# Performance work log

Measured on AMD Instinct MI355X. Metric: run time of the kernel, lower is better.

## Reference

```python
import jax, jax.numpy as jnp
import numpy as np

B, S, D_MODEL = 2, 2048, 1024
N_HEADS, N_KV_HEADS, D_HEAD = 16, 4, 64
N_GROUPS = N_HEADS // N_KV_HEADS
ATTN_SCALE = 1.0 / np.sqrt(D_HEAD)  # qk_scale_factor=1.0
LOGIT_SOFTCAP = 15.0
WINDOW = 256
N_GLOBAL = 4
EPS = 1e-8


def _l2_normalize(x):
    norm = jnp.linalg.norm(x, axis=-1, keepdims=True)
    return x / (norm + EPS)


def _apply_rope(t, cos, sin):
    # t: (B, H, S, D); cos/sin: (S, D//2)
    half = t.shape[-1] // 2
    x1, x2 = t[..., :half], t[..., half:]
    c = cos[None, None, :, :]
    s = sin[None, None, :, :]
    return jnp.concatenate([x1 * c - x2 * s, x1 * s + x2 * c], axis=-1)


def _sliding_window_mask(seq_len, window, n_global):
    q = jnp.arange(seq_len)[:, None]
    k = jnp.arange(seq_len)[None, :]
    causal = k <= q
    in_window = k > q - window
    is_global = k < n_global
    return (causal & in_window | is_global)[None, None, :, :]


def setup_inputs() -> dict:
    key = jax.random.key(0)
    ks = jax.random.split(key, 7)
    x = jax.random.normal(ks[0], (B, S, D_MODEL), dtype=jnp.float32)
    # RoPE tables from standard inverse-frequency construction
    inv_freq = 1.0 / (10000.0 ** (jnp.arange(0, D_HEAD, 2, dtype=jnp.float32) / D_HEAD))
    angles = jnp.arange(S, dtype=jnp.float32)[:, None] * inv_freq[None, :]  # (S, D_HEAD//2)
    cos = jnp.cos(angles)
    sin = jnp.sin(angles)
    # causal mask supplied by caller (TransformerLM): (1,1,S,S) bool, True = attend
    mask = (jnp.arange(S)[None, :] <= jnp.arange(S)[:, None])[None, None, :, :]
    scale_in = 1.0 / np.sqrt(D_MODEL)
    Wq = jax.random.normal(ks[1], (D_MODEL, N_HEADS * D_HEAD), dtype=jnp.float32) * scale_in
    Wk = jax.random.normal(ks[2], (D_MODEL, N_KV_HEADS * D_HEAD), dtype=jnp.float32) * scale_in
    Wv = jax.random.normal(ks[3], (D_MODEL, N_KV_HEADS * D_HEAD), dtype=jnp.float32) * scale_in
    Wo = jax.random.normal(ks[4], (N_HEADS * D_HEAD, D_MODEL), dtype=jnp.float32) * (1.0 / np.sqrt(N_HEADS * D_HEAD))
    return {"x": x, "cos": cos, "sin": sin, "mask": mask, "Wq": Wq, "Wk": Wk, "Wv": Wv, "Wo": Wo}


def reference(x, cos, sin, mask, Wq, Wk, Wv, Wo):
    Bb, Ss, _ = x.shape
    q = (x @ Wq).reshape(Bb, Ss, N_HEADS, D_HEAD).transpose(0, 2, 1, 3)      # (B,H,S,D)
    k = (x @ Wk).reshape(Bb, Ss, N_KV_HEADS, D_HEAD).transpose(0, 2, 1, 3)   # (B,Hkv,S,D)
    v = (x @ Wv).reshape(Bb, Ss, N_KV_HEADS, D_HEAD).transpose(0, 2, 1, 3)
    # QK L2 normalization (in fp32)
    q = _l2_normalize(q.astype(jnp.float32)).astype(q.dtype)
    k = _l2_normalize(k.astype(jnp.float32)).astype(k.dtype)
    # RoPE
    q = _apply_rope(q, cos, sin)
    k = _apply_rope(k, cos, sin)
    # GQA: expand kv heads
    k_exp = jnp.repeat(k, N_GROUPS, axis=1)
    v_exp = jnp.repeat(v, N_GROUPS, axis=1)
    scores = jnp.einsum('bhqd,bhkd->bhqk', q.astype(jnp.float32), k_exp.astype(jnp.float32)) * ATTN_SCALE
    scores = LOGIT_SOFTCAP * jnp.tanh(scores / LOGIT_SOFTCAP)
    window_mask = _sliding_window_mask(Ss, WINDOW, N_GLOBAL)
    combined = mask & window_mask
    scores = jnp.where(combined, scores, jnp.float32(-1e9))
    weights = jax.nn.softmax(scores, axis=-1)
    context = jnp.einsum('bhqk,bhkd->bhqd', weights, v_exp.astype(jnp.float32))
    context = context.transpose(0, 2, 1, 3).reshape(Bb, Ss, N_HEADS * D_HEAD).astype(x.dtype)
    return context @ Wo
```

## Files before the change

### kernel.cpp

```cpp
#include <hip/hip_runtime.h>
#include <hip/hip_bf16.h>

#define BATCH 2
#define SLEN 2048
#define DMODEL 1024
#define NHEADS 16
#define NKV 4
#define DHEAD 64
#define WINDOW 256
#define NGLOBAL 4

typedef __attribute__((ext_vector_type(8))) short short8;
typedef __attribute__((ext_vector_type(4))) float floatx4;

__device__ __forceinline__ ushort f2bf(float f) {
    __hip_bfloat16 h = __float2bfloat16(f);
    return *reinterpret_cast<ushort*>(&h);
}
__device__ __forceinline__ float bf2f(ushort u) {
    __hip_bfloat16 h = *reinterpret_cast<__hip_bfloat16*>(&u);
    return __bfloat162float(h);
}
__device__ __forceinline__ bool is_bf16_inputs(const uint* cosu) {
    return (cosu[0] & 0xFFFFu) != 0u;
}
__device__ __forceinline__ void gload_lds16(const ushort* g, ushort* l) {
    __builtin_amdgcn_global_load_lds(
        (const __attribute__((address_space(1))) void*)g,
        (__attribute__((address_space(3))) void*)l, 16, 0, 0);
}

__global__ __launch_bounds__(256) void cvt_inputs(const void* __restrict__ x,
                                                  const void* __restrict__ cosi,
                                                  const void* __restrict__ sini,
                                                  ushort* __restrict__ xb,
                                                  float* __restrict__ cosf,
                                                  float* __restrict__ sinf,
                                                  const uint* __restrict__ cosu)
{
    const bool isbf = is_bf16_inputs(cosu);
    if (blockIdx.y == 0) {
        size_t i = (size_t)blockIdx.x * 256 + threadIdx.x;
        size_t e = i * 8;
        if (isbf) {
            *reinterpret_cast<uint4*>(xb + e) = reinterpret_cast<const uint4*>(x)[i];
        } else {
            const float* f = reinterpret_cast<const float*>(x) + e;
            ushort o[8];
#pragma unroll
            for (int j = 0; j < 8; ++j) o[j] = f2bf(f[j]);
            *reinterpret_cast<uint4*>(xb + e) = *reinterpret_cast<uint4*>(o);
        }
    } else {
        int i = blockIdx.x * 256 + threadIdx.x;
        if (i >= 2 * SLEN * 32) return;
        const void* src = (i < SLEN * 32) ? cosi : sini;
        float* dst = (i < SLEN * 32) ? cosf : sinf;
        int e = i & (SLEN * 32 - 1);
        dst[e] = isbf ? bf2f(reinterpret_cast<const ushort*>(src)[e])
                      : reinterpret_cast<const float*>(src)[e];
    }
}

__global__ __launch_bounds__(256) void prep_weights(const void* __restrict__ Wq,
                                                    const void* __restrict__ Wk,
                                                    const void* __restrict__ Wv,
                                                    const void* __restrict__ Wo,
                                                    ushort* __restrict__ Wt,
                                                    ushort* __restrict__ Wot,
                                                    const uint* __restrict__ cosu)
{
    const bool isbf = is_bf16_inputs(cosu);
    const int z = blockIdx.z;
    const void* src; ushort* dst; int C;
    if (z == 0)      { src = Wq; dst = Wt;                        C = 1024; }
    else if (z == 1) { src = Wk; dst = Wt + (size_t)1024 * 1024;  C = 256; }
    else if (z == 2) { src = Wv; dst = Wt + (size_t)1280 * 1024;  C = 256; }
    else             { src = Wo; dst = Wot;                       C = 1024; }
    const int bx = blockIdx.x * 32;
    if (bx >= C) return;
    const int by = blockIdx.y * 32;
    __shared__ ushort t[32][33];
    const int tx = threadIdx.x & 31, ty = threadIdx.x >> 5;
#pragma unroll
    for (int j = 0; j < 32; j += 8) {
        size_t idx = (size_t)(by + ty + j) * C + bx + tx;
        t[ty + j][tx] = isbf ? reinterpret_cast<const ushort*>(src)[idx]
                             : f2bf(reinterpret_cast<const float*>(src)[idx]);
    }
    __syncthreads();
#pragma unroll
    for (int j = 0; j < 32; j += 8)
        dst[(size_t)(bx + ty + j) * 1024 + by + tx] = t[tx][ty + j];
}

__global__ __launch_bounds__(256) void transpose_slab_bf16(const ushort* __restrict__ in,
                                                           ushort* __restrict__ out,
                                                           int R, int C)
{
    __shared__ ushort t[32][33];
    const ushort* ip = in + (size_t)blockIdx.z * R * C;
    ushort* op = out + (size_t)blockIdx.z * R * C;
    int bx = blockIdx.x * 32, by = blockIdx.y * 32;
    int tx = threadIdx.x & 31, ty = threadIdx.x >> 5;
#pragma unroll
    for (int j = 0; j < 32; j += 8)
        t[ty + j][tx] = ip[(size_t)(by + ty + j) * C + bx + tx];
    __syncthreads();
#pragma unroll
    for (int j = 0; j < 32; j += 8)
        op[(size_t)(bx + ty + j) * R + by + tx] = t[tx][ty + j];
}

template<int OUT_MODE>
__global__ __launch_bounds__(256) void gemm128(const ushort* __restrict__ A,
                                               const ushort* __restrict__ Bt,
                                               void* __restrict__ Cp,
                                               int M, int N, int K,
                                               const uint* __restrict__ cosu)
{
    __shared__ ushort lsA[128 * 64];
    __shared__ ushort lsB[128 * 64];
    const int tid = threadIdx.x;
    const int lane = tid & 63, w = tid >> 6;
    const int ln15 = lane & 15, quad = lane >> 4;
    const int wm = w >> 1, wn = w & 1;
    const int rm = blockIdx.y * 128, cn = blockIdx.x * 128;

    floatx4 acc[4][4];
#pragma unroll
    for (int i = 0; i < 4; ++i)
#pragma unroll
        for (int j = 0; j < 4; ++j) acc[i][j] = (floatx4){0.f, 0.f, 0.f, 0.f};

    for (int k0 = 0; k0 < K; k0 += 64) {
        __syncthreads();
#pragma unroll
        for (int i = 0; i < 4; ++i) {
            const int c = (i * 4 + w) * 64 + lane;
            const int row = c >> 3, col = (c & 7) * 8;
            gload_lds16(&A[(size_t)(rm + row) * K + k0 + col], &lsA[(i * 4 + w) * 512]);
            gload_lds16(&Bt[(size_t)(cn + row) * K + k0 + col], &lsB[(i * 4 + w) * 512]);
        }
        __syncthreads();
#pragma unroll
        for (int kk = 0; kk < 64; kk += 32) {
            short8 af[4], bf[4];
#pragma unroll
            for (int i = 0; i < 4; ++i) {
                af[i] = *reinterpret_cast<const short8*>(&lsA[(wm * 64 + i * 16 + ln15) * 64 + kk + quad * 8]);
                bf[i] = *reinterpret_cast<const short8*>(&lsB[(wn * 64 + i * 16 + ln15) * 64 + kk + quad * 8]);
            }
#pragma unroll
            for (int i = 0; i < 4; ++i)
#pragma unroll
                for (int j = 0; j < 4; ++j)
                    acc[i][j] = __builtin_amdgcn_mfma_f32_16x16x32_bf16(af[i], bf[j], acc[i][j], 0, 0, 0);
        }
    }

    const bool outbf = (OUT_MODE == 2) || is_bf16_inputs(cosu);
#pragma unroll
    for (int i = 0; i < 4; ++i) {
#pragma unroll
        for (int r = 0; r < 4; ++r) {
            const int grow = rm + wm * 64 + i * 16 + quad * 4 + r;
#pragma unroll
            for (int j = 0; j < 4; ++j) {
                const int gcol = cn + wn * 64 + j * 16 + ln15;
                if (outbf) reinterpret_cast<ushort*>(Cp)[(size_t)grow * N + gcol] = f2bf(acc[i][j][r]);
                else       reinterpret_cast<float*>(Cp)[(size_t)grow * N + gcol] = acc[i][j][r];
            }
        }
    }
}

__global__ __launch_bounds__(256) void norm_rope(const ushort* __restrict__ qkvb,
                                                 const float* __restrict__ cosf,
                                                 const float* __restrict__ sinf,
                                                 ushort* __restrict__ Qb,
                                                 ushort* __restrict__ Kg,
                                                 ushort* __restrict__ Vb)
{
    const int lane = threadIdx.x & 63;
    const int g = blockIdx.x * 4 + (threadIdx.x >> 6);
    const int hh = g % 24;
    const int s = (g / 24) & (SLEN - 1);
    const int b = g / (24 * SLEN);
    const size_t row = (size_t)(b * SLEN + s) * 1536;

    if (hh >= 20) {
        int hkv = hh - 20;
        Vb[((size_t)((b * NKV + hkv) * SLEN + s)) * 64 + lane] = qkvb[row + 1280 + hkv * 64 + lane];
        return;
    }
    const bool isq = hh < 16;
    const int col = isq ? hh * 64 : 1024 + (hh - 16) * 64;
    float v = bf2f(qkvb[row + col + lane]);
    float ss = v * v;
#pragma unroll
    for (int off = 32; off; off >>= 1) ss += __shfl_xor(ss, off, 64);
    float nv = v / (sqrtf(ss) + 1e-8f);
    float p = __shfl(nv, lane ^ 32, 64);
    int dh = lane & 31;
    float c = cosf[s * 32 + dh];
    float sn = sinf[s * 32 + dh];
    float o = (lane < 32) ? (nv * c - p * sn) : (p * sn + nv * c);
    if (isq) Qb[((size_t)((b * NHEADS + hh) * SLEN + s)) * 64 + lane] = f2bf(o);
    else {
        int hkv = hh - 16;
        Kg[((size_t)((b * NKV + hkv) * SLEN + s)) * 64 + lane] = f2bf(o);
    }
}

__global__ __launch_bounds__(256) void attn_mfma(const ushort* __restrict__ Qb,
                                                 const ushort* __restrict__ Kg,
                                                 const ushort* __restrict__ Vtg,
                                                 ushort* __restrict__ ctx)
{
    __shared__ ushort Ks[64 * 72];
    __shared__ ushort Vs[64 * 72];
    __shared__ ushort Ps[4][16 * 72];

    const int tid = threadIdx.x;
    const int lane = tid & 63, w = tid >> 6;
    const int ln15 = lane & 15, quad = lane >> 4;
    const int bid = blockIdx.x;
    const int qt = bid & 31, bh = bid >> 5;
    const int h = bh & (NHEADS - 1), b = bh >> 4, hkv = h >> 2;
    const int q0 = qt * 64;
    const int qw = q0 + w * 16;

    const ushort* Qrow = Qb + ((size_t)bh * SLEN + qw) * 64;
    const ushort* Kbase = Kg + (size_t)(b * NKV + hkv) * SLEN * 64;
    const ushort* Vbase = Vtg + (size_t)(b * NKV + hkv) * 64 * SLEN;

    short8 qf0 = *reinterpret_cast<const short8*>(Qrow + (size_t)ln15 * 64 + quad * 8);
    short8 qf1 = *reinterpret_cast<const short8*>(Qrow + (size_t)ln15 * 64 + 32 + quad * 8);

    floatx4 O0 = {0,0,0,0}, O1 = {0,0,0,0}, O2 = {0,0,0,0}, O3 = {0,0,0,0};
    float lp[4] = {0.f, 0.f, 0.f, 0.f};

    int kminA = q0 - (WINDOW - 1); if (kminA < 0) kminA = 0;
    kminA &= ~63;
    const int gmax = kminA < NGLOBAL ? kminA : NGLOBAL;
    const int nc = (q0 + 64 - kminA) >> 6;

    for (int c = (gmax > 0 ? -1 : 0); c < nc; ++c) {
        const int kbase = (c < 0) ? 0 : kminA + c * 64;
        __syncthreads();
#pragma unroll
        for (int j = 0; j < 2; ++j) {
            const int c2 = tid + j * 256;
            const int row = c2 >> 3, col = (c2 & 7) * 8;
            *reinterpret_cast<uint4*>(&Ks[row * 72 + col]) =
                *reinterpret_cast<const uint4*>(&Kbase[(size_t)(kbase + row) * 64 + col]);
            *reinterpret_cast<uint4*>(&Vs[row * 72 + col]) =
                *reinterpret_cast<const uint4*>(&Vbase[(size_t)row * SLEN + kbase + col]);
        }
        __syncthreads();

#pragma unroll
        for (int t = 0; t < 4; ++t) {
            short8 kf0 = *reinterpret_cast<const short8*>(&Ks[(t * 16 + ln15) * 72 + quad * 8]);
            short8 kf1 = *reinterpret_cast<const short8*>(&Ks[(t * 16 + ln15) * 72 + 32 + quad * 8]);
            floatx4 sc = {0,0,0,0};
            sc = __builtin_amdgcn_mfma_f32_16x16x32_bf16(qf0, kf0, sc, 0, 0, 0);
            sc = __builtin_amdgcn_mfma_f32_16x16x32_bf16(qf1, kf1, sc, 0, 0, 0);
            const int k = kbase + t * 16 + ln15;
#pragma unroll
            for (int r = 0; r < 4; ++r) {
                const int q = qw + quad * 4 + r;
                const bool valid = (c < 0) ? (k < gmax)
                                           : (k <= q && (k + WINDOW > q || k < NGLOBAL));
                float sv = sc[r] * 0.125f;
                float e2 = __expf(sv * 0.13333333f);
                float st = 15.f - 30.f * __builtin_amdgcn_rcpf(e2 + 1.f);
                ushort eb = valid ? f2bf(__expf(st)) : (ushort)0;
                Ps[w][(quad * 4 + r) * 72 + t * 16 + ln15] = eb;
                lp[r] += bf2f(eb);
            }
        }
        short8 af0 = *reinterpret_cast<const short8*>(&Ps[w][ln15 * 72 + quad * 8]);
        short8 af1 = *reinterpret_cast<const short8*>(&Ps[w][ln15 * 72 + 32 + quad * 8]);
#pragma unroll
        for (int n = 0; n < 4; ++n) {
            short8 vf0 = *reinterpret_cast<const short8*>(&Vs[(n * 16 + ln15) * 72 + quad * 8]);
            short8 vf1 = *reinterpret_cast<const short8*>(&Vs[(n * 16 + ln15) * 72 + 32 + quad * 8]);
            floatx4 On = (n == 0) ? O0 : (n == 1) ? O1 : (n == 2) ? O2 : O3;
            On = __builtin_amdgcn_mfma_f32_16x16x32_bf16(af0, vf0, On, 0, 0, 0);
            On = __builtin_amdgcn_mfma_f32_16x16x32_bf16(af1, vf1, On, 0, 0, 0);
            if (n == 0) O0 = On; else if (n == 1) O1 = On; else if (n == 2) O2 = On; else O3 = On;
        }
    }

#pragma unroll
    for (int r = 0; r < 4; ++r) {
#pragma unroll
        for (int off = 1; off < 16; off <<= 1)
            lp[r] += __shfl_xor(lp[r], off, 64);
        const float inv = __builtin_amdgcn_rcpf(lp[r]);
        const int q = qw + quad * 4 + r;
        ushort* crow = ctx + ((size_t)(b * SLEN + q)) * DMODEL + h * 64 + ln15;
        crow[0]  = f2bf(O0[r] * inv);
        crow[16] = f2bf(O1[r] * inv);
        crow[32] = f2bf(O2[r] * inv);
        crow[48] = f2bf(O3[r] * inv);
    }
}

extern "C" void kernel_launch(void* const* d_in, const int* in_sizes, int n_in,
                              void* d_out, int out_size, void* d_ws, size_t ws_size,
                              hipStream_t stream)
{
    (void)in_sizes; (void)n_in; (void)out_size; (void)ws_size;
    const void* x = d_in[0];
    const void* cosi = d_in[1];
    const void* sini = d_in[2];
    const uint* cosu = (const uint*)d_in[1];
    const void* Wq = d_in[4];
    const void* Wk = d_in[5];
    const void* Wv = d_in[6];
    const void* Wo = d_in[7];

    ushort* xb = (ushort*)d_ws;
    ushort* Wt = xb + (size_t)4096 * 1024;
    ushort* Wot = Wt + (size_t)1536 * 1024;
    float* cosf = (float*)(Wot + (size_t)1024 * 1024);
    float* sinf = cosf + (size_t)SLEN * 32;
    ushort* qkvb = (ushort*)(sinf + (size_t)SLEN * 32);
    ushort* Qbf = qkvb + (size_t)4096 * 1536;
    ushort* Kgf = Qbf + (size_t)BATCH * NHEADS * SLEN * 64;
    ushort* Vbf = Kgf + (size_t)BATCH * NKV * SLEN * 64;
    ushort* Vtg = Vbf + (size_t)BATCH * NKV * SLEN * 64;
    ushort* ctx = Vtg + (size_t)BATCH * NKV * 64 * SLEN;

    cvt_inputs<<<dim3(2048, 2), 256, 0, stream>>>(x, cosi, sini, xb, cosf, sinf, cosu);

    prep_weights<<<dim3(32, 32, 4), 256, 0, stream>>>(Wq, Wk, Wv, Wo, Wt, Wot, cosu);

    gemm128<2><<<dim3(12, 32), 256, 0, stream>>>(xb, Wt, qkvb, 4096, 1536, 1024, cosu);

    norm_rope<<<dim3(BATCH * SLEN * 24 / 4), 256, 0, stream>>>(qkvb, cosf, sinf, Qbf, Kgf, Vbf);

    transpose_slab_bf16<<<dim3(2, 64, BATCH * NKV), 256, 0, stream>>>(Vbf, Vtg, SLEN, 64);

    attn_mfma<<<dim3(BATCH * NHEADS * SLEN / 64), 256, 0, stream>>>(Qbf, Kgf, Vtg, ctx);

    gemm128<1><<<dim3(8, 32), 256, 0, stream>>>(ctx, Wot, d_out, 4096, 1024, 1024, cosu);
}
```

Measured before the change: 192.5 us.

## Split-K both projection GEMMs into two fp32 partials and reduce downstream

Both GEMMs now split K into two halves along grid z, which doubles the block count (384→768 and 256→512) so more of the GPU's compute units are busy. Each half writes fp32 partials. The QKV partials are summed inside norm_rope, which also keeps the pre-normalisation values in fp32 instead of bf16. The output projection gets a new reduce_out kernel that adds the two partials and writes bf16 or fp32. The cost is much more fp32 memory traffic (two full partial buffers written and read) plus one extra kernel launch.

Result: slower. 196.8 us (+2.2%).

```diff
diff --git a/kernel.cpp b/kernel.cpp
--- a/kernel.cpp
+++ b/kernel.cpp
@@ -112,12 +112,10 @@
         op[(size_t)(bx + ty + j) * R + by + tx] = t[tx][ty + j];
 }
 
-template<int OUT_MODE>
-__global__ __launch_bounds__(256) void gemm128(const ushort* __restrict__ A,
-                                               const ushort* __restrict__ Bt,
-                                               void* __restrict__ Cp,
-                                               int M, int N, int K,
-                                               const uint* __restrict__ cosu)
+__global__ __launch_bounds__(256) void gemm128_sk(const ushort* __restrict__ A,
+                                                  const ushort* __restrict__ Bt,
+                                                  float* __restrict__ P,
+                                                  int M, int N, int Kh)
 {
     __shared__ ushort lsA[128 * 64];
     __shared__ ushort lsB[128 * 64];
@@ -126,6 +124,8 @@
     const int ln15 = lane & 15, quad = lane >> 4;
     const int wm = w >> 1, wn = w & 1;
     const int rm = blockIdx.y * 128, cn = blockIdx.x * 128;
+    const int kbeg = blockIdx.z * Kh;
+    float* Pz = P + (size_t)blockIdx.z * M * N;
 
     floatx4 acc[4][4];
 #pragma unroll
@@ -133,14 +133,17 @@
 #pragma unroll
         for (int j = 0; j < 4; ++j) acc[i][j] = (floatx4){0.f, 0.f, 0.f, 0.f};
 
-    for (int k0 = 0; k0 < K; k0 += 64) {
+    const size_t K = blockDim.y == 1 ? 0 : 0;
+    const int Kfull = Kh * 2;
+
+    for (int k0 = kbeg; k0 < kbeg + Kh; k0 += 64) {
         __syncthreads();
 #pragma unroll
         for (int i = 0; i < 4; ++i) {
             const int c = (i * 4 + w) * 64 + lane;
             const int row = c >> 3, col = (c & 7) * 8;
-            gload_lds16(&A[(size_t)(rm + row) * K + k0 + col], &lsA[(i * 4 + w) * 512]);
-            gload_lds16(&Bt[(size_t)(cn + row) * K + k0 + col], &lsB[(i * 4 + w) * 512]);
+            gload_lds16(&A[(size_t)(rm + row) * Kfull + k0 + col], &lsA[(i * 4 + w) * 512]);
+            gload_lds16(&Bt[(size_t)(cn + row) * Kfull + k0 + col], &lsB[(i * 4 + w) * 512]);
         }
         __syncthreads();
 #pragma unroll
@@ -159,7 +162,6 @@
         }
     }
 
-    const bool outbf = (OUT_MODE == 2) || is_bf16_inputs(cosu);
 #pragma unroll
     for (int i = 0; i < 4; ++i) {
 #pragma unroll
@@ -168,14 +170,35 @@
 #pragma unroll
             for (int j = 0; j < 4; ++j) {
                 const int gcol = cn + wn * 64 + j * 16 + ln15;
-                if (outbf) reinterpret_cast<ushort*>(Cp)[(size_t)grow * N + gcol] = f2bf(acc[i][j][r]);
-                else       reinterpret_cast<float*>(Cp)[(size_t)grow * N + gcol] = acc[i][j][r];
+                Pz[(size_t)grow * N + gcol] = acc[i][j][r];
             }
         }
     }
 }
 
-__global__ __launch_bounds__(256) void norm_rope(const ushort* __restrict__ qkvb,
+__global__ __launch_bounds__(256) void reduce_out(const float* __restrict__ P,
+                                                  void* __restrict__ out,
+                                                  size_t mn4,
+                                                  const uint* __restrict__ cosu)
+{
+    const bool isbf = is_bf16_inputs(cosu);
+    size_t i = (size_t)blockIdx.x * 256 + threadIdx.x;
+    if (i >= mn4) return;
+    const size_t mn = mn4 * 4;
+    floatx4 a = *reinterpret_cast<const floatx4*>(P + i * 4);
+    floatx4 b = *reinterpret_cast<const floatx4*>(P + mn + i * 4);
+    floatx4 s = a + b;
+    if (isbf) {
+        ushort o[4];
+#pragma unroll
+        for (int j = 0; j < 4; ++j) o[j] = f2bf(s[j]);
+        reinterpret_cast<uint2*>(out)[i] = *reinterpret_cast<uint2*>(o);
+    } else {
+        reinterpret_cast<floatx4*>(out)[i] = s;
+    }
+}
+
+__global__ __launch_bounds__(256) void norm_rope(const float* __restrict__ qkvp,
                                                  const float* __restrict__ cosf,
                                                  const float* __restrict__ sinf,
                                                  ushort* __restrict__ Qb,
@@ -188,15 +211,18 @@
     const int s = (g / 24) & (SLEN - 1);
     const int b = g / (24 * SLEN);
     const size_t row = (size_t)(b * SLEN + s) * 1536;
+    const size_t MN = (size_t)4096 * 1536;
 
     if (hh >= 20) {
         int hkv = hh - 20;
-        Vb[((size_t)((b * NKV + hkv) * SLEN + s)) * 64 + lane] = qkvb[row + 1280 + hkv * 64 + lane];
+        size_t idx = row + 1280 + hkv * 64 + lane;
+        Vb[((size_t)((b * NKV + hkv) * SLEN + s)) * 64 + lane] = f2bf(qkvp[idx] + qkvp[MN + idx]);
         return;
     }
     const bool isq = hh < 16;
     const int col = isq ? hh * 64 : 1024 + (hh - 16) * 64;
-    float v = bf2f(qkvb[row + col + lane]);
+    const size_t idx = row + col + lane;
+    float v = qkvp[idx] + qkvp[MN + idx];
     float ss = v * v;
 #pragma unroll
     for (int off = 32; off; off >>= 1) ss += __shfl_xor(ss, off, 64);
@@ -328,24 +354,27 @@
     ushort* Wot = Wt + (size_t)1536 * 1024;
     float* cosf = (float*)(Wot + (size_t)1024 * 1024);
     float* sinf = cosf + (size_t)SLEN * 32;
-    ushort* qkvb = (ushort*)(sinf + (size_t)SLEN * 32);
-    ushort* Qbf = qkvb + (size_t)4096 * 1536;
+    float* qkvp = sinf + (size_t)SLEN * 32;
+    ushort* Qbf = (ushort*)(qkvp + (size_t)2 * 4096 * 1536);
     ushort* Kgf = Qbf + (size_t)BATCH * NHEADS * SLEN * 64;
     ushort* Vbf = Kgf + (size_t)BATCH * NKV * SLEN * 64;
     ushort* Vtg = Vbf + (size_t)BATCH * NKV * SLEN * 64;
     ushort* ctx = Vtg + (size_t)BATCH * NKV * 64 * SLEN;
+    float* outp = (float*)(ctx + (size_t)4096 * 1024);
 
     cvt_inputs<<<dim3(2048, 2), 256, 0, stream>>>(x, cosi, sini, xb, cosf, sinf, cosu);
 
     prep_weights<<<dim3(32, 32, 4), 256, 0, stream>>>(Wq, Wk, Wv, Wo, Wt, Wot, cosu);
 
-    gemm128<2><<<dim3(12, 32), 256, 0, stream>>>(xb, Wt, qkvb, 4096, 1536, 1024, cosu);
-
-    norm_rope<<<dim3(BATCH * SLEN * 24 / 4), 256, 0, stream>>>(qkvb, cosf, sinf, Qbf, Kgf, Vbf);
+    gemm128_sk<<<dim3(12, 32, 2), 256, 0, stream>>>(xb, Wt, qkvp, 4096, 1536, 512);
+
+    norm_rope<<<dim3(BATCH * SLEN * 24 / 4), 256, 0, stream>>>(qkvp, cosf, sinf, Qbf, Kgf, Vbf);
 
     transpose_slab_bf16<<<dim3(2, 64, BATCH * NKV), 256, 0, stream>>>(Vbf, Vtg, SLEN, 64);
 
     attn_mfma<<<dim3(BATCH * NHEADS * SLEN / 64), 256, 0, stream>>>(Qbf, Kgf, Vtg, ctx);
 
-    gemm128<1><<<dim3(8, 32), 256, 0, stream>>>(ctx, Wot, d_out, 4096, 1024, 1024, cosu);
-}
+    gemm128_sk<<<dim3(8, 32, 2), 256, 0, stream>>>(ctx, Wot, outp, 4096, 1024, 512);
+
+    reduce_out<<<dim3(4096), 256, 0, stream>>>(outp, d_out, (size_t)4096 * 1024 / 4, cosu);
+}
```

## Fuse norm/RoPE and V transpose into QKV GEMM epilogue, merge prep kernels

Applied to the files above, without the earlier changes.

Merges the input-conversion and weight-transpose kernels into a single prep launch. The QKV GEMM now uses 128x64 tiles, so each block covers exactly one head. Its epilogue applies L2 norm and RoPE for Q/K heads and writes V directly transposed, which removes the intermediate qkv buffer and two extra kernels. The output GEMM also moves to 128x64 tiles to double block count. The cost is lower per-block reuse in the GEMMs and more staging through LDS in the epilogue.

Result: faster. 166.1 us (-13.7%).

```diff
diff --git a/kernel.cpp b/kernel.cpp
--- a/kernel.cpp
+++ b/kernel.cpp
@@ -30,17 +30,25 @@
         (__attribute__((address_space(3))) void*)l, 16, 0, 0);
 }
 
-__global__ __launch_bounds__(256) void cvt_inputs(const void* __restrict__ x,
-                                                  const void* __restrict__ cosi,
-                                                  const void* __restrict__ sini,
-                                                  ushort* __restrict__ xb,
-                                                  float* __restrict__ cosf,
-                                                  float* __restrict__ sinf,
-                                                  const uint* __restrict__ cosu)
+__global__ __launch_bounds__(256) void prep_all(const void* __restrict__ x,
+                                                const void* __restrict__ cosi,
+                                                const void* __restrict__ sini,
+                                                const void* __restrict__ Wq,
+                                                const void* __restrict__ Wk,
+                                                const void* __restrict__ Wv,
+                                                const void* __restrict__ Wo,
+                                                ushort* __restrict__ xb,
+                                                float* __restrict__ cosf,
+                                                float* __restrict__ sinf,
+                                                ushort* __restrict__ Wt,
+                                                ushort* __restrict__ Wot,
+                                                const uint* __restrict__ cosu)
 {
+    __shared__ ushort t[32][33];
     const bool isbf = is_bf16_inputs(cosu);
-    if (blockIdx.y == 0) {
-        size_t i = (size_t)blockIdx.x * 256 + threadIdx.x;
+    const int bid = blockIdx.x, tid = threadIdx.x;
+    if (bid < 2048) {
+        size_t i = (size_t)bid * 256 + tid;
         size_t e = i * 8;
         if (isbf) {
             *reinterpret_cast<uint4*>(xb + e) = reinterpret_cast<const uint4*>(x)[i];
@@ -51,37 +59,25 @@
             for (int j = 0; j < 8; ++j) o[j] = f2bf(f[j]);
             *reinterpret_cast<uint4*>(xb + e) = *reinterpret_cast<uint4*>(o);
         }
-    } else {
-        int i = blockIdx.x * 256 + threadIdx.x;
-        if (i >= 2 * SLEN * 32) return;
+        return;
+    }
+    if (bid < 2560) {
+        int i = (bid - 2048) * 256 + tid;
         const void* src = (i < SLEN * 32) ? cosi : sini;
         float* dst = (i < SLEN * 32) ? cosf : sinf;
         int e = i & (SLEN * 32 - 1);
         dst[e] = isbf ? bf2f(reinterpret_cast<const ushort*>(src)[e])
                       : reinterpret_cast<const float*>(src)[e];
-    }
-}
-
-__global__ __launch_bounds__(256) void prep_weights(const void* __restrict__ Wq,
-                                                    const void* __restrict__ Wk,
-                                                    const void* __restrict__ Wv,
-                                                    const void* __restrict__ Wo,
-                                                    ushort* __restrict__ Wt,
-                                                    ushort* __restrict__ Wot,
-                                                    const uint* __restrict__ cosu)
-{
-    const bool isbf = is_bf16_inputs(cosu);
-    const int z = blockIdx.z;
-    const void* src; ushort* dst; int C;
-    if (z == 0)      { src = Wq; dst = Wt;                        C = 1024; }
-    else if (z == 1) { src = Wk; dst = Wt + (size_t)1024 * 1024;  C = 256; }
-    else if (z == 2) { src = Wv; dst = Wt + (size_t)1280 * 1024;  C = 256; }
-    else             { src = Wo; dst = Wot;                       C = 1024; }
-    const int bx = blockIdx.x * 32;
-    if (bx >= C) return;
-    const int by = blockIdx.y * 32;
-    __shared__ ushort t[32][33];
-    const int tx = threadIdx.x & 31, ty = threadIdx.x >> 5;
+        return;
+    }
+    const void* src; ushort* dst; int C, tl;
+    if (bid < 3584)      { src = Wq; dst = Wt;                       C = 1024; tl = bid - 2560; }
+    else if (bid < 3840) { src = Wk; dst = Wt + (size_t)1024 * 1024; C = 256;  tl = bid - 3584; }
+    else if (bid < 4096) { src = Wv; dst = Wt + (size_t)1280 * 1024; C = 256;  tl = bid - 3840; }
+    else                 { src = Wo; dst = Wot;                      C = 1024; tl = bid - 4096; }
+    const int nbx = C >> 5;
+    const int bx = (tl % nbx) * 32, by = (tl / nbx) * 32;
+    const int tx = tid & 31, ty = tid >> 5;
 #pragma unroll
     for (int j = 0; j < 32; j += 8) {
         size_t idx = (size_t)(by + ty + j) * C + bx + tx;
@@ -94,122 +90,117 @@
         dst[(size_t)(bx + ty + j) * 1024 + by + tx] = t[tx][ty + j];
 }
 
-__global__ __launch_bounds__(256) void transpose_slab_bf16(const ushort* __restrict__ in,
-                                                           ushort* __restrict__ out,
-                                                           int R, int C)
+__global__ __launch_bounds__(256) void gemm_qkv_nr(const ushort* __restrict__ A,
+                                                   const ushort* __restrict__ Bt,
+                                                   const float* __restrict__ cosf,
+                                                   const float* __restrict__ sinf,
+                                                   ushort* __restrict__ Qb,
+                                                   ushort* __restrict__ Kg,
+                                                   ushort* __restrict__ Vtg)
 {
-    __shared__ ushort t[32][33];
-    const ushort* ip = in + (size_t)blockIdx.z * R * C;
-    ushort* op = out + (size_t)blockIdx.z * R * C;
-    int bx = blockIdx.x * 32, by = blockIdx.y * 32;
-    int tx = threadIdx.x & 31, ty = threadIdx.x >> 5;
-#pragma unroll
-    for (int j = 0; j < 32; j += 8)
-        t[ty + j][tx] = ip[(size_t)(by + ty + j) * C + bx + tx];
-    __syncthreads();
-#pragma unroll
-    for (int j = 0; j < 32; j += 8)
-        op[(size_t)(bx + ty + j) * R + by + tx] = t[tx][ty + j];
-}
-
-template<int OUT_MODE>
-__global__ __launch_bounds__(256) void gemm128(const ushort* __restrict__ A,
-                                               const ushort* __restrict__ Bt,
-                                               void* __restrict__ Cp,
-                                               int M, int N, int K,
-                                               const uint* __restrict__ cosu)
-{
-    __shared__ ushort lsA[128 * 64];
-    __shared__ ushort lsB[128 * 64];
+    __shared__ __align__(16) ushort buf[12288];
+    ushort* lsA = buf;
+    ushort* lsB = buf + 8192;
     const int tid = threadIdx.x;
     const int lane = tid & 63, w = tid >> 6;
     const int ln15 = lane & 15, quad = lane >> 4;
-    const int wm = w >> 1, wn = w & 1;
-    const int rm = blockIdx.y * 128, cn = blockIdx.x * 128;
-
-    floatx4 acc[4][4];
-#pragma unroll
-    for (int i = 0; i < 4; ++i)
+    const int z = blockIdx.x;
+    const int rm = blockIdx.y * 128;
+    const int cn = z * 64;
+
+    floatx4 acc[2][4];
+#pragma unroll
+    for (int i = 0; i < 2; ++i)
 #pragma unroll
         for (int j = 0; j < 4; ++j) acc[i][j] = (floatx4){0.f, 0.f, 0.f, 0.f};
 
-    for (int k0 = 0; k0 < K; k0 += 64) {
+    for (int k0 = 0; k0 < 1024; k0 += 64) {
         __syncthreads();
 #pragma unroll
         for (int i = 0; i < 4; ++i) {
             const int c = (i * 4 + w) * 64 + lane;
             const int row = c >> 3, col = (c & 7) * 8;
-            gload_lds16(&A[(size_t)(rm + row) * K + k0 + col], &lsA[(i * 4 + w) * 512]);
-            gload_lds16(&Bt[(size_t)(cn + row) * K + k0 + col], &lsB[(i * 4 + w) * 512]);
+            gload_lds16(&A[(size_t)(rm + row) * 1024 + k0 + col], &lsA[(i * 4 + w) * 512]);
+        }
+#pragma unroll
+        for (int i = 0; i < 2; ++i) {
+            const int c = (w * 2 + i) * 64 + lane;
+            const int row = c >> 3, col = (c & 7) * 8;
+            gload_lds16(&Bt[(size_t)(cn + row) * 1024 + k0 + col], &lsB[(w * 2 + i) * 512]);
         }
         __syncthreads();
 #pragma unroll
         for (int kk = 0; kk < 64; kk += 32) {
-            short8 af[4], bf[4];
-#pragma unroll
-            for (int i = 0; i < 4; ++i) {
-                af[i] = *reinterpret_cast<const short8*>(&lsA[(wm * 64 + i * 16 + ln15) * 64 + kk + quad * 8]);
-                bf[i] = *reinterpret_cast<const short8*>(&lsB[(wn * 64 + i * 16 + ln15) * 64 + kk + quad * 8]);
+            short8 af[2], bv[4];
+#pragma unroll
+            for (int i = 0; i < 2; ++i)
+                af[i] = *reinterpret_cast<const short8*>(&lsA[(w * 32 + i * 16 + ln15) * 64 + kk + quad * 8]);
+#pragma unroll
+            for (int j = 0; j < 4; ++j)
+                bv[j] = *reinterpret_cast<const short8*>(&lsB[(j * 16 + ln15) * 64 + kk + quad * 8]);
+#pragma unroll
+            for (int i = 0; i < 2; ++i)
+#pragma unroll
+                for (int j = 0; j < 4; ++j)
+                    acc[i][j] = __builtin_amdgcn_mfma_f32_16x16x32_bf16(af[i], bv[j], acc[i][j], 0, 0, 0);
+        }
+    }
+
+    __syncthreads();
+    const int b = rm >> 11, s0 = rm & (SLEN - 1);
+
+    if (z < 20) {
+#pragma unroll
+        for (int i = 0; i < 2; ++i) {
+#pragma unroll
+            for (int r = 0; r < 4; ++r) {
+                const int row_l = w * 32 + i * 16 + quad * 4 + r;
+                float v0 = acc[i][0][r], v1 = acc[i][1][r], v2 = acc[i][2][r], v3 = acc[i][3][r];
+                float ss = v0 * v0 + v1 * v1 + v2 * v2 + v3 * v3;
+                ss += __shfl_xor(ss, 1, 64);
+                ss += __shfl_xor(ss, 2, 64);
+                ss += __shfl_xor(ss, 4, 64);
+                ss += __shfl_xor(ss, 8, 64);
+                const float inv = 1.f / (sqrtf(ss) + 1e-8f);
+                const float n0 = v0 * inv, n1 = v1 * inv, n2 = v2 * inv, n3 = v3 * inv;
+                const int spos = s0 + row_l;
+                const float c0 = cosf[spos * 32 + ln15],      c1 = cosf[spos * 32 + 16 + ln15];
+                const float sn0 = sinf[spos * 32 + ln15],     sn1 = sinf[spos * 32 + 16 + ln15];
+                buf[row_l * 72 + ln15]      = f2bf(n0 * c0 - n2 * sn0);
+                buf[row_l * 72 + 16 + ln15] = f2bf(n1 * c1 - n3 * sn1);
+                buf[row_l * 72 + 32 + ln15] = f2bf(n0 * sn0 + n2 * c0);
+                buf[row_l * 72 + 48 + ln15] = f2bf(n1 * sn1 + n3 * c1);
             }
-#pragma unroll
-            for (int i = 0; i < 4; ++i)
+        }
+        __syncthreads();
+        ushort* dst = (z < 16) ? Qb + ((size_t)(b * NHEADS + z) * SLEN + s0) * 64
+                               : Kg + ((size_t)(b * NKV + (z - 16)) * SLEN + s0) * 64;
+#pragma unroll
+        for (int it = 0; it < 4; ++it) {
+            const int c = it * 256 + tid;
+            const int row = c >> 3, col = (c & 7) * 8;
+            *reinterpret_cast<uint4*>(dst + (size_t)row * 64 + col) =
+                *reinterpret_cast<const uint4*>(&buf[row * 72 + col]);
+        }
+    } else {
+#pragma unroll
+        for (int i = 0; i < 2; ++i)
+#pragma unroll
+            for (int r = 0; r < 4; ++r) {
+                const int row_l = w * 32 + i * 16 + quad * 4 + r;
 #pragma unroll
                 for (int j = 0; j < 4; ++j)
-                    acc[i][j] = __builtin_amdgcn_mfma_f32_16x16x32_bf16(af[i], bf[j], acc[i][j], 0, 0, 0);
-        }
-    }
-
-    const bool outbf = (OUT_MODE == 2) || is_bf16_inputs(cosu);
-#pragma unroll
-    for (int i = 0; i < 4; ++i) {
-#pragma unroll
-        for (int r = 0; r < 4; ++r) {
-            const int grow = rm + wm * 64 + i * 16 + quad * 4 + r;
-#pragma unroll
-            for (int j = 0; j < 4; ++j) {
-                const int gcol = cn + wn * 64 + j * 16 + ln15;
-                if (outbf) reinterpret_cast<ushort*>(Cp)[(size_t)grow * N + gcol] = f2bf(acc[i][j][r]);
-                else       reinterpret_cast<float*>(Cp)[(size_t)grow * N + gcol] = acc[i][j][r];
+                    buf[(j * 16 + ln15) * 136 + row_l] = f2bf(acc[i][j][r]);
             }
-        }
-    }
-}
-
-__global__ __launch_bounds__(256) void norm_rope(const ushort* __restrict__ qkvb,
-                                                 const float* __restrict__ cosf,
-                                                 const float* __restrict__ sinf,
-                                                 ushort* __restrict__ Qb,
-                                                 ushort* __restrict__ Kg,
-                                                 ushort* __restrict__ Vb)
-{
-    const int lane = threadIdx.x & 63;
-    const int g = blockIdx.x * 4 + (threadIdx.x >> 6);
-    const int hh = g % 24;
-    const int s = (g / 24) & (SLEN - 1);
-    const int b = g / (24 * SLEN);
-    const size_t row = (size_t)(b * SLEN + s) * 1536;
-
-    if (hh >= 20) {
-        int hkv = hh - 20;
-        Vb[((size_t)((b * NKV + hkv) * SLEN + s)) * 64 + lane] = qkvb[row + 1280 + hkv * 64 + lane];
-        return;
-    }
-    const bool isq = hh < 16;
-    const int col = isq ? hh * 64 : 1024 + (hh - 16) * 64;
-    float v = bf2f(qkvb[row + col + lane]);
-    float ss = v * v;
-#pragma unroll
-    for (int off = 32; off; off >>= 1) ss += __shfl_xor(ss, off, 64);
-    float nv = v / (sqrtf(ss) + 1e-8f);
-    float p = __shfl(nv, lane ^ 32, 64);
-    int dh = lane & 31;
-    float c = cosf[s * 32 + dh];
-    float sn = sinf[s * 32 + dh];
-    float o = (lane < 32) ? (nv * c - p * sn) : (p * sn + nv * c);
-    if (isq) Qb[((size_t)((b * NHEADS + hh) * SLEN + s)) * 64 + lane] = f2bf(o);
-    else {
-        int hkv = hh - 16;
-        Kg[((size_t)((b * NKV + hkv) * SLEN + s)) * 64 + lane] = f2bf(o);
+        __syncthreads();
+        ushort* dst = Vtg + ((size_t)(b * NKV + (z - 20)) * 64) * SLEN;
+#pragma unroll
+        for (int it = 0; it < 4; ++it) {
+            const int c = it * 256 + tid;
+            const int d = c >> 4, sb = (c & 15) * 8;
+            *reinterpret_cast<uint4*>(dst + (size_t)d * SLEN + s0 + sb) =
+                *reinterpret_cast<const uint4*>(&buf[d * 136 + sb]);
+        }
     }
 }
 
@@ -306,6 +297,74 @@
         crow[16] = f2bf(O1[r] * inv);
         crow[32] = f2bf(O2[r] * inv);
         crow[48] = f2bf(O3[r] * inv);
+    }
+}
+
+__global__ __launch_bounds__(256) void gemm_out(const ushort* __restrict__ A,
+                                                const ushort* __restrict__ Bt,
+                                                void* __restrict__ out,
+                                                const uint* __restrict__ cosu)
+{
+    __shared__ __align__(16) ushort buf[12288];
+    ushort* lsA = buf;
+    ushort* lsB = buf + 8192;
+    const int tid = threadIdx.x;
+    const int lane = tid & 63, w = tid >> 6;
+    const int ln15 = lane & 15, quad = lane >> 4;
+    const int rm = blockIdx.y * 128;
+    const int cn = blockIdx.x * 64;
+
+    floatx4 acc[2][4];
+#pragma unroll
+    for (int i = 0; i < 2; ++i)
+#pragma unroll
+        for (int j = 0; j < 4; ++j) acc[i][j] = (floatx4){0.f, 0.f, 0.f, 0.f};
+
+    for (int k0 = 0; k0 < 1024; k0 += 64) {
+        __syncthreads();
+#pragma unroll
+        for (int i = 0; i < 4; ++i) {
+            const int c = (i * 4 + w) * 64 + lane;
+            const int row = c >> 3, col = (c & 7) * 8;
+            gload_lds16(&A[(size_t)(rm + row) * 1024 + k0 + col], &lsA[(i * 4 + w) * 512]);
+        }
+#pragma unroll
+        for (int i = 0; i < 2; ++i) {
+            const int c = (w * 2 + i) * 64 + lane;
+            const int row = c >> 3, col = (c & 7) * 8;
+            gload_lds16(&Bt[(size_t)(cn + row) * 1024 + k0 + col], &lsB[(w * 2 + i) * 512]);
+        }
+        __syncthreads();
+#pragma unroll
+        for (int kk = 0; kk < 64; kk += 32) {
+            short8 af[2], bv[4];
+#pragma unroll
+            for (int i = 0; i < 2; ++i)
+                af[i] = *reinterpret_cast<const short8*>(&lsA[(w * 32 + i * 16 + ln15) * 64 + kk + quad * 8]);
+#pragma unroll
+            for (int j = 0; j < 4; ++j)
+                bv[j] = *reinterpret_cast<const short8*>(&lsB[(j * 16 + ln15) * 64 + kk + quad * 8]);
+#pragma unroll
+            for (int i = 0; i < 2; ++i)
+#pragma unroll
+                for (int j = 0; j < 4; ++j)
+                    acc[i][j] = __builtin_amdgcn_mfma_f32_16x16x32_bf16(af[i], bv[j], acc[i][j], 0, 0, 0);
+        }
+    }
+
+    const bool outbf = is_bf16_inputs(cosu);
+#pragma unroll
+    for (int i = 0; i < 2; ++i) {
+#pragma unroll
+        for (int r = 0; r < 4; ++r) {
+            const int grow = rm + w * 32 + i * 16 + quad * 4 + r;
+#pragma unroll
+            for (int j = 0; j < 4; ++j) {
+                const int gcol = cn + j * 16 + ln15;
+                if (outbf) reinterpret_cast<ushort*>(out)[(size_t)grow * DMODEL + gcol] = f2bf(acc[i][j][r]);
+                else       reinterpret_cast<float*>(out)[(size_t)grow * DMODEL + gcol] = acc[i][j][r];
+            }
+        }
     }
 }
 
@@ -328,24 +387,17 @@
     ushort* Wot = Wt + (size_t)1536 * 1024;
     float* cosf = (float*)(Wot + (size_t)1024 * 1024);
     float* sinf = cosf + (size_t)SLEN * 32;
-    ushort* qkvb = (ushort*)(sinf + (size_t)SLEN * 32);
-    ushort* Qbf = qkvb + (size_t)4096 * 1536;
+    ushort* Qbf = (ushort*)(sinf + (size_t)SLEN * 32);
     ushort* Kgf = Qbf + (size_t)BATCH * NHEADS * SLEN * 64;
-    ushort* Vbf = Kgf + (size_t)BATCH * NKV * SLEN * 64;
-    ushort* Vtg = Vbf + (size_t)BATCH * NKV * SLEN * 64;
+    ushort* Vtg = Kgf + (size_t)BATCH * NKV * SLEN * 64;
     ushort* ctx = Vtg + (size_t)BATCH * NKV * 64 * SLEN;
 
-    cvt_inputs<<<dim3(2048, 2), 256, 0, stream>>>(x, cosi, sini, xb, cosf, sinf, cosu);
-
-    prep_weights<<<dim3(32, 32, 4), 256, 0, stream>>>(Wq, Wk, Wv, Wo, Wt, Wot, cosu);
-
-    gemm128<2><<<dim3(12, 32), 256, 0, stream>>>(xb, Wt, qkvb, 4096, 1536, 1024, cosu);
-
-    norm_rope<<<dim3(BATCH * SLEN * 24 / 4), 256, 0, stream>>>(qkvb, cosf, sinf, Qbf, Kgf, Vbf);
-
-    transpose_slab_bf16<<<dim3(2, 64, BATCH * NKV), 256, 0, stream>>>(Vbf, Vtg, SLEN, 64);
+    prep_all<<<dim3(5120), 256, 0, stream>>>(x, cosi, sini, Wq, Wk, Wv, Wo,
+                                             xb, cosf, sinf, Wt, Wot, cosu);
+
+    gemm_qkv_nr<<<dim3(24, 32), 256, 0, stream>>>(xb, Wt, cosf, sinf, Qbf, Kgf, Vtg);
 
     attn_mfma<<<dim3(BATCH * NHEADS * SLEN / 64), 256, 0, stream>>>(Qbf, Kgf, Vtg, ctx);
 
-    gemm128<1><<<dim3(8, 32), 256, 0, stream>>>(ctx, Wot, d_out, 4096, 1024, 1024, cosu);
-}
+    gemm_out<<<dim3(16, 32), 256, 0, stream>>>(ctx, Wot, d_out, cosu);
+}
```
